# Optimization experiments

Hardware: AMD Instinct MI355X
Metric: run time of the kernel (lower is better)

## Reference

```python
import jax, jax.numpy as jnp
import numpy as np

NUM_HEADS = 16
THETA = 10000.0
EPS = 1e-5


def rmsnorm(x, g):
    ms = jnp.mean(x * x, axis=-1, keepdims=True)
    return x * jax.lax.rsqrt(ms + EPS) * g


def rope(x, positions, theta):
    # x: [b, h, s, dh]; rotate interleaved even/odd pairs
    dh = x.shape[-1]
    inv_freq = theta ** (-jnp.arange(0, dh, 2, dtype=jnp.float32) / dh)  # [dh/2]
    ang = positions.astype(jnp.float32)[:, None] * inv_freq[None, :]      # [s, dh/2]
    cos, sin = jnp.cos(ang), jnp.sin(ang)
    x1, x2 = x[..., 0::2], x[..., 1::2]
    r1 = x1 * cos - x2 * sin
    r2 = x1 * sin + x2 * cos
    return jnp.stack([r1, r2], axis=-1).reshape(x.shape)


def setup_inputs() -> dict:
    key = jax.random.key(0)
    ks = jax.random.split(key, 9)
    B, S, D, F = 2, 2048, 1024, 4096
    sd = 1.0 / np.sqrt(D)
    sf = 1.0 / np.sqrt(F)
    return {
        "x": jax.random.normal(ks[0], (B, S, D), dtype=jnp.float32),
        "wq": jax.random.normal(ks[1], (D, D), dtype=jnp.float32) * sd,
        "wk": jax.random.normal(ks[2], (D, D), dtype=jnp.float32) * sd,
        "wv": jax.random.normal(ks[3], (D, D), dtype=jnp.float32) * sd,
        "wo": jax.random.normal(ks[4], (D, D), dtype=jnp.float32) * sd,
        "w1": jax.random.normal(ks[5], (F, D), dtype=jnp.float32) * sd,
        "w2": jax.random.normal(ks[6], (D, F), dtype=jnp.float32) * sf,
        "w3": jax.random.normal(ks[7], (F, D), dtype=jnp.float32) * sd,
        "g1": jnp.ones((D,), dtype=jnp.float32),
        "g2": jnp.ones((D,), dtype=jnp.float32),
    }


def reference(x, wq, wk, wv, wo, w1, w2, w3, g1, g2):
    B, S, D = x.shape
    H = NUM_HEADS
    Dh = D // H
    pos = jnp.arange(S)

    # --- attention sublayer (pre-norm) ---
    h = rmsnorm(x, g1)
    # torch Linear weight is [out, in]: y = h @ w.T
    q = (h @ wq.T).reshape(B, S, H, Dh).transpose(0, 2, 1, 3)
    k = (h @ wk.T).reshape(B, S, H, Dh).transpose(0, 2, 1, 3)
    v = (h @ wv.T).reshape(B, S, H, Dh).transpose(0, 2, 1, 3)
    q = rope(q, pos, THETA)
    k = rope(k, pos, THETA)

    scores = jnp.einsum("bhqd,bhkd->bhqk", q, k) / jnp.sqrt(jnp.float32(Dh))
    causal = jnp.tril(jnp.ones((S, S), dtype=bool))
    scores = jnp.where(causal, scores, jnp.finfo(scores.dtype).min)
    attn = jax.nn.softmax(scores, axis=-1)
    o = jnp.einsum("bhqk,bhkd->bhqd", attn, v)
    o = o.transpose(0, 2, 1, 3).reshape(B, S, D) @ wo.T
    x = x + o

    # --- SwiGLU FFN sublayer (pre-norm) ---
    h2 = rmsnorm(x, g2)
    ff = (jax.nn.silu(h2 @ w1.T) * (h2 @ w3.T)) @ w2.T
    return x + ff
```

## Files before the change

### kernel.cpp

```cpp
#include <hip/hip_runtime.h>


typedef unsigned short u16;
typedef __attribute__((ext_vector_type(8))) short short8;
typedef __attribute__((ext_vector_type(4))) float f32x4;

#define MBYTE ((size_t)1 << 20)

typedef void __attribute__((address_space(3))) lds_void;
typedef void __attribute__((address_space(1))) glb_void;
#define GLD_LDS16(gp, lp) \
  __builtin_amdgcn_global_load_lds((glb_void*)(gp), (lds_void*)(lp), 16, 0, 0)

__device__ __forceinline__ u16 f2bf(float f) {
  union { float f; unsigned u; } v; v.f = f;
  unsigned r = v.u + 0x7FFFu + ((v.u >> 16) & 1u);
  return (u16)(r >> 16);
}
__device__ __forceinline__ float bf2f(u16 h) {
  union { unsigned u; float f; } v; v.u = ((unsigned)h) << 16;
  return v.f;
}

__global__ __launch_bounds__(256)
void prep_kernel(const float* __restrict__ wq, const float* __restrict__ wk,
                 const float* __restrict__ wv, const float* __restrict__ wo,
                 const float* __restrict__ w1, const float* __restrict__ w2,
                 const float* __restrict__ w3,
                 u16* wqb, u16* wkb, u16* wvb, u16* wob,
                 u16* w1b, u16* w2b, u16* w3b, float2* trig)
{
  const int y = blockIdx.y;
  if (y == 7) {
    const int idx = blockIdx.x * 256 + threadIdx.x;
    if (idx < 2048 * 32) {
      const int s = idx >> 5, i = idx & 31;
      const float inv = powf(10000.0f, -(float)(2 * i) / 64.0f);
      const float ang = (float)s * inv;
      trig[idx] = make_float2(cosf(ang), sinf(ang));
    }
    return;
  }
  const float* src; u16* dst; int n;
  switch (y) {
    case 0: src = wq; dst = wqb; n = 1 << 20; break;
    case 1: src = wk; dst = wkb; n = 1 << 20; break;
    case 2: src = wv; dst = wvb; n = 1 << 20; break;
    case 3: src = wo; dst = wob; n = 1 << 20; break;
    case 4: src = w1; dst = w1b; n = 1 << 22; break;
    case 5: src = w2; dst = w2b; n = 1 << 22; break;
    default: src = w3; dst = w3b; n = 1 << 22; break;
  }
  const int idx = (blockIdx.x * 256 + threadIdx.x) * 4;
  if (idx >= n) return;
  const float4 v = *(const float4*)(src + idx);
  ushort4 o; o.x = f2bf(v.x); o.y = f2bf(v.y); o.z = f2bf(v.z); o.w = f2bf(v.w);
  *(ushort4*)(dst + idx) = o;
}

__global__ __launch_bounds__(256)
void rmsnorm_kernel(const float* __restrict__ x, const float* __restrict__ g,
                    u16* __restrict__ out)
{
  __shared__ float red[4];
  const int row = blockIdx.x, tid = threadIdx.x;
  const float4 v = ((const float4*)(x + (size_t)row * 1024))[tid];
  float ss = v.x * v.x + v.y * v.y + v.z * v.z + v.w * v.w;
  #pragma unroll
  for (int off = 32; off >= 1; off >>= 1) ss += __shfl_xor(ss, off, 64);
  if ((tid & 63) == 0) red[tid >> 6] = ss;
  __syncthreads();
  const float tot = red[0] + red[1] + red[2] + red[3];
  const float rs = rsqrtf(tot * (1.0f / 1024.0f) + 1e-5f);
  const float4 gg = ((const float4*)g)[tid];
  ushort4 o;
  o.x = f2bf(v.x * rs * gg.x); o.y = f2bf(v.y * rs * gg.y);
  o.z = f2bf(v.z * rs * gg.z); o.w = f2bf(v.w * rs * gg.w);
  ((ushort4*)(out + (size_t)row * 1024))[tid] = o;
}

template<int TM, int TN, int WRN, int WCN>
__device__ __forceinline__ void gemm_core(const u16* __restrict__ A,
                                          const u16* __restrict__ Bw,
                                          int K, int bm, int bn,
                                          u16* As, u16* Bs,
                                          f32x4 (&acc)[TM / (16 * WRN)][TN / (16 * WCN)])
{
  constexpr int MT = TM / (16 * WRN), NT = TN / (16 * WCN);
  constexpr int CA = TM / 16, CB = TN / 16;
  const int tid = threadIdx.x, wid = tid >> 6, lane = tid & 63;
  const int wr = wid / WCN, wc = wid % WCN;
  const int lr = lane & 15, lg = lane >> 4;
  const int srow = lane >> 2;
  const int skel = (lane & 3) * 8;
  const size_t aRow0 = (size_t)bm * TM;
  const size_t bRow0 = (size_t)bn * TN;

  for (int k0 = 0; k0 < K; k0 += 32) {
    #pragma unroll
    for (int i = 0; i < CA / 4; i++) {
      int c = wid + i * 4;
      GLD_LDS16(A + (aRow0 + c * 16 + srow) * K + k0 + skel, As + c * 512);
    }
    #pragma unroll
    for (int i = 0; i < CB / 4; i++) {
      int c = wid + i * 4;
      GLD_LDS16(Bw + (bRow0 + c * 16 + srow) * K + k0 + skel, Bs + c * 512);
    }
    __syncthreads();
    short8 af[MT], bfr[NT];
    #pragma unroll
    for (int mt = 0; mt < MT; mt++)
      af[mt] = *(const short8*)&As[(wr * (MT * 16) + mt * 16 + lr) * 32 + lg * 8];
    #pragma unroll
    for (int nt = 0; nt < NT; nt++)
      bfr[nt] = *(const short8*)&Bs[(wc * (NT * 16) + nt * 16 + lr) * 32 + lg * 8];
    #pragma unroll
    for (int mt = 0; mt < MT; mt++)
      #pragma unroll
      for (int nt = 0; nt < NT; nt++)
        acc[mt][nt] = __builtin_amdgcn_mfma_f32_16x16x32_bf16(af[mt], bfr[nt],
                                                              acc[mt][nt], 0, 0, 0);
    __syncthreads();
  }
}

__global__ __launch_bounds__(256)
void gemm_qkv(const u16* __restrict__ A,
              const u16* __restrict__ wqb, const u16* __restrict__ wkb,
              const u16* __restrict__ wvb,
              u16* Qb, u16* Kb, u16* Vb, const float2* __restrict__ trig)
{
  __shared__ u16 As[128 * 32];
  __shared__ u16 Bs[128 * 32];
  const u16* Bw = blockIdx.z == 0 ? wqb : (blockIdx.z == 1 ? wkb : wvb);
  u16* out = blockIdx.z == 0 ? Qb : (blockIdx.z == 1 ? Kb : Vb);
  const bool isQK = blockIdx.z < 2;
  f32x4 acc[4][4];
  const f32x4 zero = {0.f, 0.f, 0.f, 0.f};
  #pragma unroll
  for (int i = 0; i < 4; i++)
    #pragma unroll
    for (int j = 0; j < 4; j++) acc[i][j] = zero;
  gemm_core<128, 128, 2, 2>(A, Bw, 1024, blockIdx.y, blockIdx.x, As, Bs, acc);
  const int lane = threadIdx.x & 63, wid = threadIdx.x >> 6;
  const int wr = wid >> 1, wc = wid & 1, lr = lane & 15, lg = lane >> 4;
  #pragma unroll
  for (int mt = 0; mt < 4; mt++)
    #pragma unroll
    for (int nt = 0; nt < 4; nt++)
      #pragma unroll
      for (int j = 0; j < 4; j++) {
        int row = blockIdx.y * 128 + wr * 64 + mt * 16 + lg * 4 + j;
        int col = blockIdx.x * 128 + wc * 64 + nt * 16 + lr;
        int b = row >> 11, s = row & 2047, hh = col >> 6, d = col & 63;
        float v = acc[mt][nt][j];
        if (isQK) {
          float p = __shfl_xor(v, 1);
          const float2 cs = trig[s * 32 + (d >> 1)];
          v = ((d & 1) == 0) ? (v * cs.x - p * cs.y)
                             : (p * cs.y + v * cs.x);
        }
        out[(((size_t)(b * 16 + hh)) * 2048 + s) * 64 + d] = f2bf(v);
      }
}

template<int EP, int TM, int TN, int WRN, int WCN>
__global__ __launch_bounds__(256)
void gemm_one(const u16* __restrict__ A, const u16* __restrict__ Bw, int K, int N,
              u16* outb, float* outf, const float* res)
{
  __shared__ u16 As[TM * 32];
  __shared__ u16 Bs[TN * 32];
  constexpr int MT = TM / (16 * WRN), NT = TN / (16 * WCN);
  f32x4 acc[MT][NT];
  const f32x4 zero = {0.f, 0.f, 0.f, 0.f};
  #pragma unroll
  for (int i = 0; i < MT; i++)
    #pragma unroll
    for (int j = 0; j < NT; j++) acc[i][j] = zero;
  gemm_core<TM, TN, WRN, WCN>(A, Bw, K, blockIdx.y, blockIdx.x, As, Bs, acc);
  const int lane = threadIdx.x & 63, wid = threadIdx.x >> 6;
  const int wr = wid / WCN, wc = wid % WCN, lr = lane & 15, lg = lane >> 4;
  #pragma unroll
  for (int mt = 0; mt < MT; mt++)
    #pragma unroll
    for (int nt = 0; nt < NT; nt++)
      #pragma unroll
      for (int j = 0; j < 4; j++) {
        int row = blockIdx.y * TM + wr * (MT * 16) + mt * 16 + lg * 4 + j;
        int col = blockIdx.x * TN + wc * (NT * 16) + nt * 16 + lr;
        size_t o = (size_t)row * N + col;
        float v = acc[mt][nt][j];
        if constexpr (EP == 1) {
          outb[o] = f2bf(v);
        } else {
          outf[o] = res[o] + v;
        }
      }
}

__global__ __launch_bounds__(256)
void gemm_ffn13(const u16* __restrict__ A, const u16* __restrict__ W1,
                const u16* __restrict__ W3, u16* __restrict__ outb)
{
  __shared__ u16 As[128 * 32];
  __shared__ u16 B1s[64 * 32];
  __shared__ u16 B3s[64 * 32];
  f32x4 acc1[4][2], acc3[4][2];
  const f32x4 zero = {0.f, 0.f, 0.f, 0.f};
  #pragma unroll
  for (int i = 0; i < 4; i++)
    #pragma unroll
    for (int j = 0; j < 2; j++) { acc1[i][j] = zero; acc3[i][j] = zero; }
  const int tid = threadIdx.x, wid = tid >> 6, lane = tid & 63;
  const int wr = wid >> 1, wc = wid & 1;
  const int lr = lane & 15, lg = lane >> 4;
  const int srow = lane >> 2;
  const int skel = (lane & 3) * 8;
  const size_t aRow0 = (size_t)blockIdx.y * 128;
  const size_t bRow0 = (size_t)blockIdx.x * 64;

  for (int k0 = 0; k0 < 1024; k0 += 32) {
    #pragma unroll
    for (int i = 0; i < 2; i++) {
      int c = wid + i * 4;
      GLD_LDS16(A + (aRow0 + c * 16 + srow) * 1024 + k0 + skel, As + c * 512);
    }
    GLD_LDS16(W1 + (bRow0 + wid * 16 + srow) * 1024 + k0 + skel, B1s + wid * 512);
    GLD_LDS16(W3 + (bRow0 + wid * 16 + srow) * 1024 + k0 + skel, B3s + wid * 512);
    __syncthreads();
    short8 af[4], b1[2], b3[2];
    #pragma unroll
    for (int mt = 0; mt < 4; mt++)
      af[mt] = *(const short8*)&As[(wr * 64 + mt * 16 + lr) * 32 + lg * 8];
    #pragma unroll
    for (int nt = 0; nt < 2; nt++) {
      b1[nt] = *(const short8*)&B1s[(wc * 32 + nt * 16 + lr) * 32 + lg * 8];
      b3[nt] = *(const short8*)&B3s[(wc * 32 + nt * 16 + lr) * 32 + lg * 8];
    }
    #pragma unroll
    for (int mt = 0; mt < 4; mt++)
      #pragma unroll
      for (int nt = 0; nt < 2; nt++) {
        acc1[mt][nt] = __builtin_amdgcn_mfma_f32_16x16x32_bf16(af[mt], b1[nt],
                                                               acc1[mt][nt], 0, 0, 0);
        acc3[mt][nt] = __builtin_amdgcn_mfma_f32_16x16x32_bf16(af[mt], b3[nt],
                                                               acc3[mt][nt], 0, 0, 0);
      }
    __syncthreads();
  }
  #pragma unroll
  for (int mt = 0; mt < 4; mt++)
    #pragma unroll
    for (int nt = 0; nt < 2; nt++)
      #pragma unroll
      for (int j = 0; j < 4; j++) {
        int row = blockIdx.y * 128 + wr * 64 + mt * 16 + lg * 4 + j;
        int col = blockIdx.x * 64 + wc * 32 + nt * 16 + lr;
        float v1 = acc1[mt][nt][j], v3 = acc3[mt][nt][j];
        float sg = v1 / (1.0f + __expf(-v1));
        outb[(size_t)row * 4096 + col] = f2bf(sg * v3);
      }
}

__global__ __launch_bounds__(256)
void flash_attn(const u16* __restrict__ Qb, const u16* __restrict__ Kb,
                const u16* __restrict__ Vb, u16* __restrict__ Ob)
{
  __shared__ u16 Ks[2][64 * 64];
  __shared__ u16 Vt[2][64 * 64];
  __shared__ u16 Ps[4 * 16 * 72];
  const int tid = threadIdx.x, wid = tid >> 6, lane = tid & 63;
  const int lr = lane & 15, lg = lane >> 4;
  const int bh = blockIdx.y;
  const int qt = (blockIdx.x + blockIdx.y) & 31;
  const size_t base = (size_t)bh * (2048 * 64);

  short8 qf[2];
  #pragma unroll
  for (int kc = 0; kc < 2; kc++)
    qf[kc] = *(const short8*)&Qb[base + (size_t)(qt * 64 + wid * 16 + lr) * 64
                                 + kc * 32 + lg * 8];

  f32x4 oacc[4];
  float mrow[4], lrow[4];
  const f32x4 zero = {0.f, 0.f, 0.f, 0.f};
  #pragma unroll
  for (int d = 0; d < 4; d++) oacc[d] = zero;
  #pragma unroll
  for (int j = 0; j < 4; j++) { mrow[j] = -1e30f; lrow[j] = 0.0f; }

  short8 vv[2];
  #pragma unroll
  for (int c = 0; c < 2; c++) {
    int ci = (wid * 2 + c) * 64 + lane;
    int row = ci >> 3;
    int lch = (ci & 7) ^ (row & 7);
    GLD_LDS16(Kb + base + (size_t)(row)*64 + lch * 8, (u16*)Ks[0] + (wid * 2 + c) * 512);
  }
  #pragma unroll
  for (int c = 0; c < 2; c++)
    vv[c] = *(const short8*)&Vb[base + (size_t)lane * 64 + (c * 4 + wid) * 8];
  asm volatile("s_waitcnt vmcnt(0)" ::: "memory");
  #pragma unroll
  for (int c = 0; c < 2; c++)
    #pragma unroll
    for (int j = 0; j < 8; j++) {
      int d = (c * 4 + wid) * 8 + j;
      int byt = d * 128 + (((lane >> 3) ^ (d & 7)) << 4) + ((lane & 7) << 1);
      *(u16*)((char*)Vt[0] + byt) = (u16)vv[c][j];
    }
  __syncthreads();

  int buf = 0;
  for (int kt = 0; kt <= qt; kt++) {
    if (kt < qt) {
      #pragma unroll
      for (int c = 0; c < 2; c++) {
        int ci = (wid * 2 + c) * 64 + lane;
        int row = ci >> 3;
        int lch = (ci & 7) ^ (row & 7);
        GLD_LDS16(Kb + base + (size_t)((kt + 1) * 64 + row) * 64 + lch * 8,
                  (u16*)Ks[buf ^ 1] + (wid * 2 + c) * 512);
      }
      #pragma unroll
      for (int c = 0; c < 2; c++)
        vv[c] = *(const short8*)&Vb[base + (size_t)((kt + 1) * 64 + lane) * 64
                                    + (c * 4 + wid) * 8];
    }

    f32x4 sv[4];
    #pragma unroll
    for (int nt = 0; nt < 4; nt++) {
      f32x4 s = zero;
      #pragma unroll
      for (int kc = 0; kc < 2; kc++) {
        int row = nt * 16 + lr;
        int pch = (kc * 4 + lg) ^ (row & 7);
        short8 kf = *(const short8*)((const char*)Ks[buf] + row * 128 + pch * 16);
        s = __builtin_amdgcn_mfma_f32_16x16x32_bf16(qf[kc], kf, s, 0, 0, 0);
      }
      s *= 0.125f;
      if (kt == qt) {
        int key = kt * 64 + nt * 16 + lr;
        #pragma unroll
        for (int j = 0; j < 4; j++) {
          int q = qt * 64 + wid * 16 + lg * 4 + j;
          if (key > q) s[j] = -1e30f;
        }
      }
      sv[nt] = s;
    }

    #pragma unroll
    for (int j = 0; j < 4; j++) {
      float tm = fmaxf(fmaxf(sv[0][j], sv[1][j]), fmaxf(sv[2][j], sv[3][j]));
      #pragma unroll
      for (int off = 8; off >= 1; off >>= 1) tm = fmaxf(tm, __shfl_xor(tm, off, 64));
      float mnew = fmaxf(mrow[j], tm);
      float esc = __expf(mrow[j] - mnew);
      mrow[j] = mnew;
      float rs = 0.f;
      #pragma unroll
      for (int nt = 0; nt < 4; nt++) {
        float p = __expf(sv[nt][j] - mnew);
        sv[nt][j] = p;
        rs += p;
      }
      #pragma unroll
      for (int off = 8; off >= 1; off >>= 1) rs += __shfl_xor(rs, off, 64);
      lrow[j] = lrow[j] * esc + rs;
      #pragma unroll
      for (int dt = 0; dt < 4; dt++) oacc[dt][j] *= esc;
    }

    u16* myP = (u16*)Ps + wid * (16 * 72);
    #pragma unroll
    for (int nt = 0; nt < 4; nt++)
      #pragma unroll
      for (int j = 0; j < 4; j++)
        myP[(lg * 4 + j) * 72 + nt * 16 + lr] = f2bf(sv[nt][j]);
    asm volatile("s_waitcnt lgkmcnt(0)" ::: "memory");
    short8 pa[2];
    #pragma unroll
    for (int kc = 0; kc < 2; kc++)
      pa[kc] = *(const short8*)&myP[lr * 72 + kc * 32 + lg * 8];

    #pragma unroll
    for (int dt = 0; dt < 4; dt++) {
      #pragma unroll
      for (int kc = 0; kc < 2; kc++) {
        int d = dt * 16 + lr;
        int pch = (kc * 4 + lg) ^ (d & 7);
        short8 vf = *(const short8*)((const char*)Vt[buf] + d * 128 + pch * 16);
        oacc[dt] = __builtin_amdgcn_mfma_f32_16x16x32_bf16(pa[kc], vf, oacc[dt], 0, 0, 0);
      }
    }

    if (kt < qt) {
      asm volatile("s_waitcnt vmcnt(0)" ::: "memory");
      #pragma unroll
      for (int c = 0; c < 2; c++)
        #pragma unroll
        for (int j = 0; j < 8; j++) {
          int d = (c * 4 + wid) * 8 + j;
          int byt = d * 128 + (((lane >> 3) ^ (d & 7)) << 4) + ((lane & 7) << 1);
          *(u16*)((char*)Vt[buf ^ 1] + byt) = (u16)vv[c][j];
        }
    }
    __syncthreads();
    buf ^= 1;
  }

  const int b = bh >> 4, h = bh & 15;
  #pragma unroll
  for (int dt = 0; dt < 4; dt++)
    #pragma unroll
    for (int j = 0; j < 4; j++) {
      int sq = qt * 64 + wid * 16 + lg * 4 + j;
      Ob[((size_t)(b * 2048 + sq)) * 1024 + h * 64 + dt * 16 + lr] =
          f2bf(oacc[dt][j] / lrow[j]);
    }
}

extern "C" void kernel_launch(void* const* d_in, const int* in_sizes, int n_in,
                              void* d_out, int out_size, void* d_ws, size_t ws_size,
                              hipStream_t stream)
{
  const float* x  = (const float*)d_in[0];
  const float* wq = (const float*)d_in[1];
  const float* wk = (const float*)d_in[2];
  const float* wv = (const float*)d_in[3];
  const float* wo = (const float*)d_in[4];
  const float* w1 = (const float*)d_in[5];
  const float* w2 = (const float*)d_in[6];
  const float* w3 = (const float*)d_in[7];
  const float* g1 = (const float*)d_in[8];
  const float* g2 = (const float*)d_in[9];
  float* out = (float*)d_out;
  char* ws = (char*)d_ws;

  u16*    wqb  = (u16*)   (ws + 0 * MBYTE);
  u16*    wkb  = (u16*)   (ws + 2 * MBYTE);
  u16*    wvb  = (u16*)   (ws + 4 * MBYTE);
  u16*    wob  = (u16*)   (ws + 6 * MBYTE);
  u16*    w1b  = (u16*)   (ws + 8 * MBYTE);
  u16*    w2b  = (u16*)   (ws + 16 * MBYTE);
  u16*    w3b  = (u16*)   (ws + 24 * MBYTE);
  float2* trig = (float2*)(ws + 32 * MBYTE);
  float*  x2   = (float*) (ws + 33 * MBYTE);
  u16*    hb   = (u16*)   (ws + 49 * MBYTE);
  u16*    Qb   = (u16*)   (ws + 57 * MBYTE);
  u16*    Kb   = (u16*)   (ws + 65 * MBYTE);
  u16*    Vb   = (u16*)   (ws + 73 * MBYTE);
  u16*    Ob   = (u16*)   (ws + 81 * MBYTE);
  u16*    f1   = (u16*)   (ws + 57 * MBYTE);

  prep_kernel<<<dim3(4096, 8), 256, 0, stream>>>(wq, wk, wv, wo, w1, w2, w3,
                                                 wqb, wkb, wvb, wob, w1b, w2b, w3b,
                                                 trig);
  rmsnorm_kernel<<<4096, 256, 0, stream>>>(x, g1, hb);
  gemm_qkv<<<dim3(8, 32, 3), 256, 0, stream>>>(hb, wqb, wkb, wvb, Qb, Kb, Vb, trig);
  flash_attn<<<dim3(32, 32), 256, 0, stream>>>(Qb, Kb, Vb, Ob);
  gemm_one<2, 64, 128, 1, 4><<<dim3(8, 64), 256, 0, stream>>>(
      Ob, wob, 1024, 1024, nullptr, x2, x);
  rmsnorm_kernel<<<4096, 256, 0, stream>>>(x2, g2, hb);
  gemm_ffn13<<<dim3(64, 32), 256, 0, stream>>>(hb, w1b, w3b, f1);
  gemm_one<2, 64, 128, 1, 4><<<dim3(8, 64), 256, 0, stream>>>(
      f1, w2b, 4096, 1024, nullptr, out, x2);
}
```

Before: 497.8 us.

## Pair complementary causal query tiles per flash-attention block to balance work

Each flash-attention block now handles two query tiles, qtA and 31-qtA, so every block does the same total number of key tiles under the causal mask. The shared K/V tiles loaded for the longer tile are reused by the shorter one, which halves redundant K/V loads for early tiles. The grid is halved to 512 blocks. In exchange there are fewer blocks to fill the GPU, and register pressure roughly doubles for the accumulators, which may reduce occupancy.

```diff
diff --git a/kernel.cpp b/kernel.cpp
--- a/kernel.cpp
+++ b/kernel.cpp
@@ -274,22 +274,100 @@
   const int tid = threadIdx.x, wid = tid >> 6, lane = tid & 63;
   const int lr = lane & 15, lg = lane >> 4;
   const int bh = blockIdx.y;
-  const int qt = (blockIdx.x + blockIdx.y) & 31;
+  const int qtA = blockIdx.x;
+  const int qtB = 31 - qtA;
   const size_t base = (size_t)bh * (2048 * 64);
-
-  short8 qf[2];
-  #pragma unroll
-  for (int kc = 0; kc < 2; kc++)
-    qf[kc] = *(const short8*)&Qb[base + (size_t)(qt * 64 + wid * 16 + lr) * 64
-                                 + kc * 32 + lg * 8];
-
-  f32x4 oacc[4];
-  float mrow[4], lrow[4];
   const f32x4 zero = {0.f, 0.f, 0.f, 0.f};
-  #pragma unroll
-  for (int d = 0; d < 4; d++) oacc[d] = zero;
-  #pragma unroll
-  for (int j = 0; j < 4; j++) { mrow[j] = -1e30f; lrow[j] = 0.0f; }
+
+  short8 qfA[2], qfB[2];
+  #pragma unroll
+  for (int kc = 0; kc < 2; kc++) {
+    qfA[kc] = *(const short8*)&Qb[base + (size_t)(qtA * 64 + wid * 16 + lr) * 64
+                                  + kc * 32 + lg * 8];
+    qfB[kc] = *(const short8*)&Qb[base + (size_t)(qtB * 64 + wid * 16 + lr) * 64
+                                  + kc * 32 + lg * 8];
+  }
+
+  f32x4 oaccA[4], oaccB[4];
+  float mrowA[4], lrowA[4], mrowB[4], lrowB[4];
+  #pragma unroll
+  for (int d = 0; d < 4; d++) { oaccA[d] = zero; oaccB[d] = zero; }
+  #pragma unroll
+  for (int j = 0; j < 4; j++) {
+    mrowA[j] = -1e30f; lrowA[j] = 0.0f;
+    mrowB[j] = -1e30f; lrowB[j] = 0.0f;
+  }
+
+  auto process = [&](int kt, int qtX, const short8 (&qf)[2], f32x4 (&oacc)[4],
+                     float (&mrow)[4], float (&lrow)[4], int buf) {
+    f32x4 sv[4];
+    #pragma unroll
+    for (int nt = 0; nt < 4; nt++) {
+      f32x4 s = zero;
+      #pragma unroll
+      for (int kc = 0; kc < 2; kc++) {
+        int row = nt * 16 + lr;
+        int pch = (kc * 4 + lg) ^ (row & 7);
+        short8 kf = *(const short8*)((const char*)Ks[buf] + row * 128 + pch * 16);
+        s = __builtin_amdgcn_mfma_f32_16x16x32_bf16(qf[kc], kf, s, 0, 0, 0);
+      }
+      s *= 0.125f;
+      if (kt == qtX) {
+        int key = kt * 64 + nt * 16 + lr;
+        #pragma unroll
+        for (int j = 0; j < 4; j++) {
+          int q = qtX * 64 + wid * 16 + lg * 4 + j;
+          if (key > q) s[j] = -1e30f;
+        }
+      }
+      sv[nt] = s;
+    }
+
+    #pragma unroll
+    for (int j = 0; j < 4; j++) {
+      float tm = fmaxf(fmaxf(sv[0][j], sv[1][j]), fmaxf(sv[2][j], sv[3][j]));
+      #pragma unroll
+      for (int off = 8; off >= 1; off >>= 1) tm = fmaxf(tm, __shfl_xor(tm, off, 64));
+      float mnew = fmaxf(mrow[j], tm);
+      float esc = __expf(mrow[j] - mnew);
+      mrow[j] = mnew;
+      float rs = 0.f;
+      #pragma unroll
+      for (int nt = 0; nt < 4; nt++) {
+        float p = __expf(sv[nt][j] - mnew);
+        sv[nt][j] = p;
+        rs += p;
+      }
+      #pragma unroll
+      for (int off = 8; off >= 1; off >>= 1) rs += __shfl_xor(rs, off, 64);
+      lrow[j] = lrow[j] * esc + rs;
+      #pragma unroll
+      for (int dt = 0; dt < 4; dt++) oacc[dt][j] *= esc;
+    }
+
+    u16* myP = (u16*)Ps + wid * (16 * 72);
+    #pragma unroll
+    for (int nt = 0; nt < 4; nt++)
+      #pragma unroll
+      for (int j = 0; j < 4; j++)
+        myP[(lg * 4 + j) * 72 + nt * 16 + lr] = f2bf(sv[nt][j]);
+    asm volatile("s_waitcnt lgkmcnt(0)" ::: "memory");
+    short8 pa[2];
+    #pragma unroll
+    for (int kc = 0; kc < 2; kc++)
+      pa[kc] = *(const short8*)&myP[lr * 72 + kc * 32 + lg * 8];
+
+    #pragma unroll
+    for (int dt = 0; dt < 4; dt++) {
+      #pragma unroll
+      for (int kc = 0; kc < 2; kc++) {
+        int d = dt * 16 + lr;
+        int pch = (kc * 4 + lg) ^ (d & 7);
+        short8 vf = *(const short8*)((const char*)Vt[buf] + d * 128 + pch * 16);
+        oacc[dt] = __builtin_amdgcn_mfma_f32_16x16x32_bf16(pa[kc], vf, oacc[dt], 0, 0, 0);
+      }
+    }
+  };
 
   short8 vv[2];
   #pragma unroll
@@ -314,8 +392,8 @@
   __syncthreads();
 
   int buf = 0;
-  for (int kt = 0; kt <= qt; kt++) {
-    if (kt < qt) {
+  for (int kt = 0; kt <= qtB; kt++) {
+    if (kt < qtB) {
       #pragma unroll
       for (int c = 0; c < 2; c++) {
         int ci = (wid * 2 + c) * 64 + lane;
@@ -330,75 +408,11 @@
                                     + (c * 4 + wid) * 8];
     }
 
-    f32x4 sv[4];
-    #pragma unroll
-    for (int nt = 0; nt < 4; nt++) {
-      f32x4 s = zero;
-      #pragma unroll
-      for (int kc = 0; kc < 2; kc++) {
-        int row = nt * 16 + lr;
-        int pch = (kc * 4 + lg) ^ (row & 7);
-        short8 kf = *(const short8*)((const char*)Ks[buf] + row * 128 + pch * 16);
-        s = __builtin_amdgcn_mfma_f32_16x16x32_bf16(qf[kc], kf, s, 0, 0, 0);
-      }
-      s *= 0.125f;
-      if (kt == qt) {
-        int key = kt * 64 + nt * 16 + lr;
-        #pragma unroll
-        for (int j = 0; j < 4; j++) {
-          int q = qt * 64 + wid * 16 + lg * 4 + j;
-          if (key > q) s[j] = -1e30f;
-        }
-      }
-      sv[nt] = s;
-    }
-
-    #pragma unroll
-    for (int j = 0; j < 4; j++) {
-      float tm = fmaxf(fmaxf(sv[0][j], sv[1][j]), fmaxf(sv[2][j], sv[3][j]));
-      #pragma unroll
-      for (int off = 8; off >= 1; off >>= 1) tm = fmaxf(tm, __shfl_xor(tm, off, 64));
-      float mnew = fmaxf(mrow[j], tm);
-      float esc = __expf(mrow[j] - mnew);
-      mrow[j] = mnew;
-      float rs = 0.f;
-      #pragma unroll
-      for (int nt = 0; nt < 4; nt++) {
-        float p = __expf(sv[nt][j] - mnew);
-        sv[nt][j] = p;
-        rs += p;
-      }
-      #pragma unroll
-      for (int off = 8; off >= 1; off >>= 1) rs += __shfl_xor(rs, off, 64);
-      lrow[j] = lrow[j] * esc + rs;
-      #pragma unroll
-      for (int dt = 0; dt < 4; dt++) oacc[dt][j] *= esc;
-    }
-
-    u16* myP = (u16*)Ps + wid * (16 * 72);
-    #pragma unroll
-    for (int nt = 0; nt < 4; nt++)
-      #pragma unroll
-      for (int j = 0; j < 4; j++)
-        myP[(lg * 4 + j) * 72 + nt * 16 + lr] = f2bf(sv[nt][j]);
-    asm volatile("s_waitcnt lgkmcnt(0)" ::: "memory");
-    short8 pa[2];
-    #pragma unroll
-    for (int kc = 0; kc < 2; kc++)
-      pa[kc] = *(const short8*)&myP[lr * 72 + kc * 32 + lg * 8];
-
-    #pragma unroll
-    for (int dt = 0; dt < 4; dt++) {
-      #pragma unroll
-      for (int kc = 0; kc < 2; kc++) {
-        int d = dt * 16 + lr;
-        int pch = (kc * 4 + lg) ^ (d & 7);
-        short8 vf = *(const short8*)((const char*)Vt[buf] + d * 128 + pch * 16);
-        oacc[dt] = __builtin_amdgcn_mfma_f32_16x16x32_bf16(pa[kc], vf, oacc[dt], 0, 0, 0);
-      }
-    }
-
-    if (kt < qt) {
+    if (kt <= qtA)
+      process(kt, qtA, qfA, oaccA, mrowA, lrowA, buf);
+    process(kt, qtB, qfB, oaccB, mrowB, lrowB, buf);
+
+    if (kt < qtB) {
       asm volatile("s_waitcnt vmcnt(0)" ::: "memory");
       #pragma unroll
       for (int c = 0; c < 2; c++)
@@ -418,9 +432,12 @@
   for (int dt = 0; dt < 4; dt++)
     #pragma unroll
     for (int j = 0; j < 4; j++) {
-      int sq = qt * 64 + wid * 16 + lg * 4 + j;
-      Ob[((size_t)(b * 2048 + sq)) * 1024 + h * 64 + dt * 16 + lr] =
-          f2bf(oacc[dt][j] / lrow[j]);
+      int sqA = qtA * 64 + wid * 16 + lg * 4 + j;
+      int sqB = qtB * 64 + wid * 16 + lg * 4 + j;
+      Ob[((size_t)(b * 2048 + sqA)) * 1024 + h * 64 + dt * 16 + lr] =
+          f2bf(oaccA[dt][j] / lrowA[j]);
+      Ob[((size_t)(b * 2048 + sqB)) * 1024 + h * 64 + dt * 16 + lr] =
+          f2bf(oaccB[dt][j] / lrowB[j]);
     }
 }
 
@@ -462,7 +479,7 @@
                                                  trig);
   rmsnorm_kernel<<<4096, 256, 0, stream>>>(x, g1, hb);
   gemm_qkv<<<dim3(8, 32, 3), 256, 0, stream>>>(hb, wqb, wkb, wvb, Qb, Kb, Vb, trig);
-  flash_attn<<<dim3(32, 32), 256, 0, stream>>>(Qb, Kb, Vb, Ob);
+  flash_attn<<<dim3(16, 32), 256, 0, stream>>>(Qb, Kb, Vb, Ob);
   gemm_one<2, 64, 128, 1, 4><<<dim3(8, 64), 256, 0, stream>>>(
       Ob, wob, 1024, 1024, nullptr, x2, x);
   rmsnorm_kernel<<<4096, 256, 0, stream>>>(x2, g2, hb);
```

New measurement: 483.7 us. -2.8%, faster.
